# Performance work log

Measured on AMD Instinct MI355X. Metric: run time of the kernel, lower is better.

## Reference

```python
import jax, jax.numpy as jnp
import numpy as np

V, D, H, B, LK, LQ, PAD = 10000, 300, 512, 16, 64, 64, 0


def _lstm(x, Wih, Whh, b, h0, c0):
    # x: [B,T,D]; Wih: [4G,D]; Whh: [4G,G]; b: [4G] (b_ih+b_hh); torch gate order i,f,g,o
    xg = jnp.einsum('btd,gd->btg', x, Wih) + b
    def step(hc, xt):
        h, c = hc
        g = xt + h @ Whh.T
        i, f, gg, o = jnp.split(g, 4, axis=-1)
        c = jax.nn.sigmoid(f) * c + jax.nn.sigmoid(i) * jnp.tanh(gg)
        h = jax.nn.sigmoid(o) * jnp.tanh(c)
        return (h, c), h
    (hT, cT), hs = jax.lax.scan(step, (h0, c0), jnp.swapaxes(xg, 0, 1))
    return jnp.swapaxes(hs, 0, 1), hT, cT


def setup_inputs() -> dict:
    key = jax.random.key(0)
    ks = jax.random.split(key, 24)
    n = lambda k, s: (jax.random.normal(k, s, jnp.float32) * 0.05)
    return {
        'source': jax.random.randint(ks[0], (B, LK), 0, V),
        'prev_outputs': jax.random.randint(ks[1], (B, LQ), 0, V),
        'emb': n(ks[2], (V, D)),
        'enc_f_Wih': n(ks[3], (4 * H, D)), 'enc_f_Whh': n(ks[4], (4 * H, H)), 'enc_f_b': n(ks[5], (4 * H,)),
        'enc_b_Wih': n(ks[6], (4 * H, D)), 'enc_b_Whh': n(ks[7], (4 * H, H)), 'enc_b_b': n(ks[8], (4 * H,)),
        'dec_Wih': n(ks[9], (8 * H, D)), 'dec_Whh': n(ks[10], (8 * H, 2 * H)), 'dec_b': n(ks[11], (8 * H,)),
        'k_W': n(ks[12], (2 * H, 2 * H)), 'k_b': n(ks[13], (2 * H,)),
        'v_W': n(ks[14], (2 * H, 2 * H)), 'v_b': n(ks[15], (2 * H,)),
        'fc1_W': n(ks[16], (2 * H, 4 * H)), 'fc1_b': n(ks[17], (2 * H,)),
        'fc2_W': n(ks[18], (V, 2 * H)), 'fc2_b': n(ks[19], (V,)),
    }


def reference(source, prev_outputs, emb, enc_f_Wih, enc_f_Whh, enc_f_b,
              enc_b_Wih, enc_b_Whh, enc_b_b, dec_Wih, dec_Whh, dec_b,
              k_W, k_b, v_W, v_b, fc1_W, fc1_b, fc2_W, fc2_b):
    bsz = source.shape[0]
    xs = emb[source]  # [B,LK,300]
    z = jnp.zeros((bsz, H), xs.dtype)
    out_f, hf, cf = _lstm(xs, enc_f_Wih, enc_f_Whh, enc_f_b, z, z)
    out_b, hb, cb = _lstm(xs[:, ::-1], enc_b_Wih, enc_b_Whh, enc_b_b, z, z)
    enc_out = jnp.concatenate([out_f, out_b[:, ::-1]], axis=-1)  # [B,LK,1024]
    # self.change: interleave fwd/bwd channels -> [B,1024]
    h0 = jnp.stack([hf, hb], axis=-1).reshape(bsz, 2 * H)
    c0 = jnp.stack([cf, cb], axis=-1).reshape(bsz, 2 * H)
    Q, _, _ = _lstm(emb[prev_outputs], dec_Wih, dec_Whh, dec_b, h0, c0)  # [B,LQ,1024]
    K = enc_out @ k_W.T + k_b
    Vv = enc_out @ v_W.T + v_b
    M = jnp.einsum('bqc,bkc->bqk', Q, K)
    mask = (source == PAD)[:, None, :]
    M = jnp.where(mask, -jnp.inf, M)
    A = jax.nn.softmax(M, axis=2)
    ctx = jnp.einsum('bqk,bkc->bqc', A, Vv)  # == (A[...,None]*V[:,None]).sum(2)
    x = jnp.tanh(jnp.concatenate([ctx, Q], axis=-1) @ fc1_W.T + fc1_b)  # dropout=identity (eval)
    return x @ fc2_W.T + fc2_b
```

## Files before the change

kernel.cpp:

```cpp
#include <hip/hip_runtime.h>
#include <cmath>

#define BB   16
#define LKK  64
#define LQQ  64
#define DD   300
#define HH   512
#define H2   1024
#define G4   2048
#define G8   4096
#define VV   10000

__device__ __forceinline__ float sigmoidf_(float x) { return 1.f / (1.f + expf(-x)); }

typedef __attribute__((ext_vector_type(4))) float    f4_;
typedef __attribute__((ext_vector_type(4))) unsigned u4_;
typedef __attribute__((ext_vector_type(2))) unsigned u2_;

__device__ __forceinline__ void st_sc(float* p, float v) {
    __hip_atomic_store(p, v, __ATOMIC_RELAXED, __HIP_MEMORY_SCOPE_AGENT);
}

__device__ __forceinline__ f4_ ld4_sc(const float* p) {
    f4_ r;
    asm volatile("global_load_dwordx4 %0, %1, off sc0 sc1" : "=v"(r) : "v"(p));
    return r;
}
__device__ __forceinline__ u4_ ld4u_sc(const unsigned* p) {
    u4_ r;
    asm volatile("global_load_dwordx4 %0, %1, off sc0 sc1" : "=v"(r) : "v"(p));
    return r;
}
__device__ __forceinline__ u2_ ld2u_sc(const unsigned* p) {
    u2_ r;
    asm volatile("global_load_dwordx2 %0, %1, off sc0 sc1" : "=v"(r) : "v"(p));
    return r;
}
__device__ __forceinline__ void wait_vm0() {
    asm volatile("s_waitcnt vmcnt(0)" ::: "memory");
    __builtin_amdgcn_sched_barrier(0);
}
__device__ __forceinline__ void wait_vm1() {
    asm volatile("s_waitcnt vmcnt(1)" ::: "memory");
    __builtin_amdgcn_sched_barrier(0);
}

__device__ __forceinline__ void gbar256(unsigned* flags, int wg, unsigned target) {
    asm volatile("s_waitcnt vmcnt(0)" ::: "memory");
    if (threadIdx.x == 0)
        __hip_atomic_store(&flags[wg], target, __ATOMIC_RELAXED, __HIP_MEMORY_SCOPE_AGENT);
    if (threadIdx.x < 64) {
        const unsigned* p = flags + (threadIdx.x << 2);
        u4_ f0 = ld4u_sc(p);
        for (;;) {
            u4_ f1 = ld4u_sc(p);
            wait_vm1();
            unsigned m0 = f0[0] < f0[1] ? f0[0] : f0[1];
            unsigned m1 = f0[2] < f0[3] ? f0[2] : f0[3];
            if (__all((int)((m0 < m1 ? m0 : m1) >= target))) break;
            u4_ f2 = ld4u_sc(p);
            wait_vm1();
            m0 = f1[0] < f1[1] ? f1[0] : f1[1];
            m1 = f1[2] < f1[3] ? f1[2] : f1[3];
            if (__all((int)((m0 < m1 ? m0 : m1) >= target))) break;
            f0 = f2;
        }
        wait_vm0();
    }
    __syncthreads();
}

__device__ __forceinline__ void gbar128(unsigned* flags, int wg, unsigned target) {
    asm volatile("s_waitcnt vmcnt(0)" ::: "memory");
    if (threadIdx.x == 0)
        __hip_atomic_store(&flags[wg], target, __ATOMIC_RELAXED, __HIP_MEMORY_SCOPE_AGENT);
    if (threadIdx.x < 64) {
        const unsigned* p = flags + (threadIdx.x << 1);
        u2_ f0 = ld2u_sc(p);
        for (;;) {
            u2_ f1 = ld2u_sc(p);
            wait_vm1();
            unsigned mn = f0[0] < f0[1] ? f0[0] : f0[1];
            if (__all((int)(mn >= target))) break;
            u2_ f2 = ld2u_sc(p);
            wait_vm1();
            mn = f1[0] < f1[1] ? f1[0] : f1[1];
            if (__all((int)(mn >= target))) break;
            f0 = f2;
        }
        wait_vm0();
    }
    __syncthreads();
}

__global__ void rev_idx_kernel(const int* __restrict__ src, int* __restrict__ rev,
                               unsigned* __restrict__ bars) {
    int tid = blockIdx.x * blockDim.x + threadIdx.x;
    if (tid < 512) bars[tid] = 0u;
    if (tid < BB * LKK) {
        int b = tid / LKK, t = tid % LKK;
        rev[tid] = src[b * LKK + (LKK - 1 - t)];
    }
}

typedef __attribute__((ext_vector_type(8))) short bfrag8;
typedef __attribute__((ext_vector_type(4))) float facc4;

__device__ __forceinline__ unsigned short f2bf(float x) {
    unsigned u = __float_as_uint(x);
    unsigned r = (u + 0x7fffu + ((u >> 16) & 1u)) >> 16;
    return (unsigned short)r;
}

#define ASTR 40

__device__ __forceinline__ void gemm_core(
        short* __restrict__ Ah, short* __restrict__ Al,
        short* __restrict__ Bh, short* __restrict__ Bl,
        const float* __restrict__ A, const int* __restrict__ gidx, int lda,
        const float* __restrict__ Bw, int ldb,
        const float* __restrict__ bias,
        float* __restrict__ C, int ldc,
        int N, int K, int act, int m0, int n0) {
    int tid = threadIdx.x;
    int lane = tid & 63, w = tid >> 6;
    int wr = w >> 1, wc = w & 1;
    int fr = lane & 15, fg = lane >> 4;

    int sr = tid >> 1, sc = (tid & 1) << 4;
    long abase = gidx ? (long)gidx[m0 + sr] * lda : (long)(m0 + sr) * lda;
    int gn = n0 + sr;
    bool bval = gn < N;
    long bbase = (long)gn * ldb;

    facc4 acc[4][4] = {};

    for (int k0 = 0; k0 < K; k0 += 32) {
        {
            float v[16];
            if (k0 + sc + 16 <= K) {
                const float* ap = A + abase + k0 + sc;
                float4 t0 = *(const float4*)(ap + 0);
                float4 t1 = *(const float4*)(ap + 4);
                float4 t2 = *(const float4*)(ap + 8);
                float4 t3 = *(const float4*)(ap + 12);
                v[0]=t0.x; v[1]=t0.y; v[2]=t0.z;  v[3]=t0.w;
                v[4]=t1.x; v[5]=t1.y; v[6]=t1.z;  v[7]=t1.w;
                v[8]=t2.x; v[9]=t2.y; v[10]=t2.z; v[11]=t2.w;
                v[12]=t3.x; v[13]=t3.y; v[14]=t3.z; v[15]=t3.w;
            } else {
#pragma unroll
                for (int c = 0; c < 16; c++) {
                    int k = k0 + sc + c;
                    v[c] = (k < K) ? A[abase + k] : 0.f;
                }
            }
            bfrag8 h0, h1, l0, l1;
#pragma unroll
            for (int c = 0; c < 8; c++) {
                unsigned short hb = f2bf(v[c]);
                float hf = __uint_as_float(((unsigned)hb) << 16);
                h0[c] = (short)hb; l0[c] = (short)f2bf(v[c] - hf);
            }
#pragma unroll
            for (int c = 0; c < 8; c++) {
                unsigned short hb = f2bf(v[8 + c]);
                float hf = __uint_as_float(((unsigned)hb) << 16);
                h1[c] = (short)hb; l1[c] = (short)f2bf(v[8 + c] - hf);
            }
            *(bfrag8*)&Ah[sr * ASTR + sc]     = h0;
            *(bfrag8*)&Ah[sr * ASTR + sc + 8] = h1;
            *(bfrag8*)&Al[sr * ASTR + sc]     = l0;
            *(bfrag8*)&Al[sr * ASTR + sc + 8] = l1;
        }
        {
            float v[16];
            if (bval && (k0 + sc + 16 <= K)) {
                const float* bp = Bw + bbase + k0 + sc;
                float4 t0 = *(const float4*)(bp + 0);
                float4 t1 = *(const float4*)(bp + 4);
                float4 t2 = *(const float4*)(bp + 8);
                float4 t3 = *(const float4*)(bp + 12);
                v[0]=t0.x; v[1]=t0.y; v[2]=t0.z;  v[3]=t0.w;
                v[4]=t1.x; v[5]=t1.y; v[6]=t1.z;  v[7]=t1.w;
                v[8]=t2.x; v[9]=t2.y; v[10]=t2.z; v[11]=t2.w;
                v[12]=t3.x; v[13]=t3.y; v[14]=t3.z; v[15]=t3.w;
            } else {
#pragma unroll
                for (int c = 0; c < 16; c++) {
                    int k = k0 + sc + c;
                    v[c] = (bval && k < K) ? Bw[bbase + k] : 0.f;
                }
            }
            bfrag8 h0, h1, l0, l1;
#pragma unroll
            for (int c = 0; c < 8; c++) {
                unsigned short hb = f2bf(v[c]);
                float hf = __uint_as_float(((unsigned)hb) << 16);
                h0[c] = (short)hb; l0[c] = (short)f2bf(v[c] - hf);
            }
#pragma unroll
            for (int c = 0; c < 8; c++) {
                unsigned short hb = f2bf(v[8 + c]);
                float hf = __uint_as_float(((unsigned)hb) << 16);
                h1[c] = (short)hb; l1[c] = (short)f2bf(v[8 + c] - hf);
            }
            *(bfrag8*)&Bh[sr * ASTR + sc]     = h0;
            *(bfrag8*)&Bh[sr * ASTR + sc + 8] = h1;
            *(bfrag8*)&Bl[sr * ASTR + sc]     = l0;
            *(bfrag8*)&Bl[sr * ASTR + sc + 8] = l1;
        }
        __syncthreads();

        bfrag8 ah[4], al[4], bh[4], bl[4];
#pragma unroll
        for (int i = 0; i < 4; i++) {
            int ar = wr * 64 + i * 16 + fr;
            ah[i] = *(const bfrag8*)&Ah[ar * ASTR + fg * 8];
            al[i] = *(const bfrag8*)&Al[ar * ASTR + fg * 8];
            int br = wc * 64 + i * 16 + fr;
            bh[i] = *(const bfrag8*)&Bh[br * ASTR + fg * 8];
            bl[i] = *(const bfrag8*)&Bl[br * ASTR + fg * 8];
        }
#pragma unroll
        for (int i = 0; i < 4; i++)
#pragma unroll
            for (int j = 0; j < 4; j++) {
                acc[i][j] = __builtin_amdgcn_mfma_f32_16x16x32_bf16(ah[i], bh[j], acc[i][j], 0, 0, 0);
                acc[i][j] = __builtin_amdgcn_mfma_f32_16x16x32_bf16(ah[i], bl[j], acc[i][j], 0, 0, 0);
                acc[i][j] = __builtin_amdgcn_mfma_f32_16x16x32_bf16(al[i], bh[j], acc[i][j], 0, 0, 0);
            }
        __syncthreads();
    }

#pragma unroll
    for (int i = 0; i < 4; i++) {
        int row = m0 + wr * 64 + i * 16 + fg * 4;
#pragma unroll
        for (int j = 0; j < 4; j++) {
            int col = n0 + wc * 64 + j * 16 + fr;
            if (col < N) {
                float bz = bias[col];
#pragma unroll
                for (int q = 0; q < 4; q++) {
                    float vv = acc[i][j][q] + bz;
                    if (act == 1) vv = tanhf(vv);
                    C[(long)(row + q) * ldc + col] = vv;
                }
            }
        }
    }
}

__global__ __launch_bounds__(256)
void gemm_mfma128(const float* __restrict__ A, const int* __restrict__ gidx, int lda,
                  const float* __restrict__ Bw, int ldb,
                  const float* __restrict__ bias,
                  float* __restrict__ C, int ldc,
                  int N, int K, int act) {
    __shared__ __align__(16) short Ah[128 * ASTR];
    __shared__ __align__(16) short Al[128 * ASTR];
    __shared__ __align__(16) short Bh[128 * ASTR];
    __shared__ __align__(16) short Bl[128 * ASTR];
    gemm_core(Ah, Al, Bh, Bl, A, gidx, lda, Bw, ldb, bias, C, ldc, N, K, act,
              blockIdx.x * 128, blockIdx.y * 128);
}

__global__ __launch_bounds__(256)
void gemm_kv(const float* __restrict__ enc_out,
             const float* __restrict__ kW, const float* __restrict__ kb,
             const float* __restrict__ vW, const float* __restrict__ vb,
             float* __restrict__ Kbuf, float* __restrict__ Vbuf) {
    __shared__ __align__(16) short Ah[128 * ASTR];
    __shared__ __align__(16) short Al[128 * ASTR];
    __shared__ __align__(16) short Bh[128 * ASTR];
    __shared__ __align__(16) short Bl[128 * ASTR];
    int ny = blockIdx.y;
    if (ny < 8)
        gemm_core(Ah, Al, Bh, Bl, enc_out, nullptr, H2, kW, H2, kb, Kbuf, H2,
                  H2, H2, 0, blockIdx.x * 128, ny * 128);
    else
        gemm_core(Ah, Al, Bh, Bl, enc_out, nullptr, H2, vW, H2, vb, Vbuf, H2,
                  H2, H2, 0, blockIdx.x * 128, (ny - 8) * 128);
}

__global__ __launch_bounds__(256)
void gemm_xg(const float* __restrict__ emb,
             const int* __restrict__ src, const int* __restrict__ rev,
             const int* __restrict__ prev,
             const float* __restrict__ Wf, const float* __restrict__ bf,
             const float* __restrict__ Wb, const float* __restrict__ bb,
             const float* __restrict__ Wd, const float* __restrict__ bd,
             float* __restrict__ xf, float* __restrict__ xb,
             float* __restrict__ xd) {
    __shared__ __align__(16) short Ah[128 * ASTR];
    __shared__ __align__(16) short Al[128 * ASTR];
    __shared__ __align__(16) short Bh[128 * ASTR];
    __shared__ __align__(16) short Bl[128 * ASTR];
    int ny = blockIdx.y;
    if (ny < 16)
        gemm_core(Ah, Al, Bh, Bl, emb, src, DD, Wf, DD, bf, xf, G4,
                  G4, DD, 0, blockIdx.x * 128, ny * 128);
    else if (ny < 32)
        gemm_core(Ah, Al, Bh, Bl, emb, rev, DD, Wb, DD, bb, xb, G4,
                  G4, DD, 0, blockIdx.x * 128, (ny - 16) * 128);
    else
        gemm_core(Ah, Al, Bh, Bl, emb, prev, DD, Wd, DD, bd, xd, G8,
                  G8, DD, 0, blockIdx.x * 128, (ny - 32) * 128);
}

__global__ __launch_bounds__(256, 1)
void enc_recur(const float* __restrict__ xg_f, const float* __restrict__ xg_b,
               const float* __restrict__ Wf, const float* __restrict__ Wb,
               float* __restrict__ hglob, float* __restrict__ enc_out,
               float* __restrict__ encc, unsigned* __restrict__ flags) {
    __shared__ float hs[HH * 16];
    __shared__ float red[256 * 33];
    __shared__ float g256[256];
    __shared__ float hout[64];
    int wg  = blockIdx.x;
    int dir = wg >> 7;
    int j0  = (wg & 127) * 4;
    int tid = threadIdx.x;
    int ks   = tid & 31;
    int tile = tid >> 5;
    int bh   = tile >> 2;
    int gate = tile & 3;
    int sw   = (ks >> 2) & 3;
    const float* W  = dir ? Wb : Wf;
    const float* xg = dir ? xg_b : xg_f;
    unsigned* fl = flags + (dir << 7);
    int wgl = wg & 127;

    float wreg[4][16];
#pragma unroll
    for (int jn = 0; jn < 4; jn++) {
        const float* wrow = W + (long)(gate * HH + j0 + jn) * HH;
#pragma unroll
        for (int j = 0; j < 16; j++) wreg[jn][j] = wrow[ks + 32 * j];
    }

    int ub = tid & 15, ujj = tid >> 4;
    int xb = tid >> 4, xgate = (tid >> 2) & 3, xjn = tid & 3;
    float creg = 0.f;
    float4* hsv = (float4*)hs;

    for (int t = 0; t < LKK; t++) {
        float acc[8][4];
#pragma unroll
        for (int i = 0; i < 8; i++)
#pragma unroll
            for (int jn = 0; jn < 4; jn++) acc[i][jn] = 0.f;

        auto do_fma = [&](int jlo, int jhi) {
#pragma unroll
            for (int j = jlo; j < jhi; j++) {
                int k = ks + 32 * j;
                float4 h0 = hsv[k * 4 + ((bh * 2 + 0) ^ sw)];
                float4 h1 = hsv[k * 4 + ((bh * 2 + 1) ^ sw)];
#pragma unroll
                for (int jn = 0; jn < 4; jn++) {
                    float w = wreg[jn][j];
                    acc[0][jn] += h0.x * w; acc[1][jn] += h0.y * w;
                    acc[2][jn] += h0.z * w; acc[3][jn] += h0.w * w;
                    acc[4][jn] += h1.x * w; acc[5][jn] += h1.y * w;
                    acc[6][jn] += h1.z * w; acc[7][jn] += h1.w * w;
                }
            }
        };

        float xval = xg[(long)(xb * LKK + t) * G4 + xgate * HH + j0 + xjn];

        if (t == 0) {
            for (int i = tid; i < HH * 16; i += 256) hs[i] = 0.f;
            __syncthreads();
            do_fma(0, 16);
        } else {
            const float* hg = hglob + (long)((dir << 1) | (t & 1)) * (HH * 16);
            f4_ vv[8];
#pragma unroll
            for (int u = 0; u < 8; u++) vv[u] = ld4_sc(hg + tid * 4 + u * 1024);
            asm volatile("s_waitcnt vmcnt(4)" ::: "memory");
            __builtin_amdgcn_sched_barrier(0);
#pragma unroll
            for (int u = 0; u < 4; u++) {
                int e = tid * 4 + u * 1024;
                int jj = e >> 4, b0 = e & 15;
                *(f4_*)&hs[(jj << 4) + ((((b0 >> 2) ^ ((jj >> 2) & 3))) << 2)] = vv[u];
            }
            __syncthreads();
            do_fma(0, 8);
            wait_vm0();
#pragma unroll
            for (int u = 4; u < 8; u++) {
                int e = tid * 4 + u * 1024;
                int jj = e >> 4, b0 = e & 15;
                *(f4_*)&hs[(jj << 4) + ((((b0 >> 2) ^ ((jj >> 2) & 3))) << 2)] = vv[u];
            }
            __syncthreads();
            do_fma(8, 16);
        }

#pragma unroll
        for (int i = 0; i < 8; i++)
#pragma unroll
            for (int jn = 0; jn < 4; jn++)
                red[((bh * 8 + i) * 16 + gate * 4 + jn) * 33 + ks] = acc[i][jn];
        __syncthreads();
        {
            const float* row = red + tid * 33;
            float s0 = 0.f, s1 = 0.f, s2 = 0.f, s3 = 0.f;
#pragma unroll
            for (int u = 0; u < 8; u++) {
                s0 += row[u * 4 + 0]; s1 += row[u * 4 + 1];
                s2 += row[u * 4 + 2]; s3 += row[u * 4 + 3];
            }
            g256[tid] = ((s0 + s1) + (s2 + s3)) + xval;
        }
        __syncthreads();

        if (tid < 64) {
            int j = j0 + ujj;
            float gi = g256[ub * 16 + 0  + ujj];
            float gf = g256[ub * 16 + 4  + ujj];
            float gg = g256[ub * 16 + 8  + ujj];
            float go = g256[ub * 16 + 12 + ujj];
            float cv = sigmoidf_(gf) * creg + sigmoidf_(gi) * tanhf(gg);
            creg = cv;
            float hv = sigmoidf_(go) * tanhf(cv);
            st_sc(&hglob[(long)((dir << 1) | ((t + 1) & 1)) * (HH * 16) + j * 16 + ub], hv);
            hout[tid] = hv;
            if (t == LKK - 1) encc[(dir * BB + ub) * HH + j] = creg;
        }
        if (t < LKK - 1) gbar128(fl, wgl, (unsigned)(t + 1));
        else __syncthreads();
        if (tid >= 64 && tid < 128) {
            int lt = tid - 64;
            int j = j0 + (lt >> 4);
            int kpos = dir ? (LKK - 1 - t) : t;
            enc_out[(long)((lt & 15) * LKK + kpos) * H2 + dir * HH + j] = hout[lt];
        }
    }
}

__global__ __launch_bounds__(256, 1)
void dec_recur(const float* __restrict__ xg_d, const float* __restrict__ Wd,
               const float* __restrict__ enc_out, const float* __restrict__ encc,
               float* __restrict__ hglob, float* __restrict__ Qout,
               unsigned* __restrict__ flags) {
    __shared__ float hs[HH * 16];
    __shared__ float red[256 * 33];
    __shared__ float g256[256];
    __shared__ float hout[64];
    int wg  = blockIdx.x;
    int j0  = wg * 4;
    int tid = threadIdx.x;
    int ks   = tid & 31;
    int tile = tid >> 5;
    int bh   = tile >> 2;
    int gate = tile & 3;
    int sw   = (ks >> 2) & 3;

    float wreg[4][32];
#pragma unroll
    for (int jn = 0; jn < 4; jn++) {
        const float* wrow = Wd + (long)(gate * H2 + j0 + jn) * H2;
#pragma unroll
        for (int j = 0; j < 32; j++) wreg[jn][j] = wrow[ks + 32 * j];
    }

    int ub = tid & 15, ujj = tid >> 4;
    int xb = tid >> 4, xgate = (tid >> 2) & 3, xjn = tid & 3;
    float creg = 0.f;
    if (tid < 64) {
        int j = j0 + ujj;
        creg = ((j & 1) == 0) ? encc[ub * HH + (j >> 1)]
                              : encc[(BB + ub) * HH + (j >> 1)];
    }
    float4* hsv = (float4*)hs;

    for (int t = 0; t < LQQ; t++) {
        float xval = xg_d[(long)(xb * LQQ + t) * G8 + xgate * H2 + j0 + xjn];
        float acc[8][4];
#pragma unroll
        for (int i = 0; i < 8; i++)
#pragma unroll
            for (int jn = 0; jn < 4; jn++) acc[i][jn] = 0.f;

        auto do_fma = [&](int half) {
#pragma unroll
            for (int jj2 = 0; jj2 < 16; jj2++) {
                int j = half * 16 + jj2;
                int kl = ks + 32 * jj2;
                float4 h0 = hsv[kl * 4 + ((bh * 2 + 0) ^ sw)];
                float4 h1 = hsv[kl * 4 + ((bh * 2 + 1) ^ sw)];
#pragma unroll
                for (int jn = 0; jn < 4; jn++) {
                    float w = wreg[jn][j];
                    acc[0][jn] += h0.x * w; acc[1][jn] += h0.y * w;
                    acc[2][jn] += h0.z * w; acc[3][jn] += h0.w * w;
                    acc[4][jn] += h1.x * w; acc[5][jn] += h1.y * w;
                    acc[6][jn] += h1.z * w; acc[7][jn] += h1.w * w;
                }
            }
        };

        if (t == 0) {
            for (int half = 0; half < 2; half++) {
                for (int e = tid; e < HH * 16; e += 256) {
                    int kl = e >> 4, b = e & 15;
                    int k = half * HH + kl;
                    float hv = ((k & 1) == 0)
                        ? enc_out[(long)(b * LKK + (LKK - 1)) * H2 + (k >> 1)]
                        : enc_out[(long)(b * LKK) * H2 + HH + (k >> 1)];
                    hs[(kl << 4) + ((((b >> 2) ^ ((kl >> 2) & 3))) << 2) + (b & 3)] = hv;
                }
                __syncthreads();
                do_fma(half);
                __syncthreads();
            }
        } else {
            const float* hgA = hglob + (long)(t & 1) * (H2 * 16);
            f4_ vvA[8], vvB[8];
#pragma unroll
            for (int u = 0; u < 8; u++) vvA[u] = ld4_sc(hgA + tid * 4 + u * 1024);
#pragma unroll
            for (int u = 0; u < 8; u++) vvB[u] = ld4_sc(hgA + (HH * 16) + tid * 4 + u * 1024);
            asm volatile("s_waitcnt vmcnt(8)" ::: "memory");
            __builtin_amdgcn_sched_barrier(0);
#pragma unroll
            for (int u = 0; u < 8; u++) {
                int e = tid * 4 + u * 1024;
                int kl = e >> 4, b0 = e & 15;
                *(f4_*)&hs[(kl << 4) + ((((b0 >> 2) ^ ((kl >> 2) & 3))) << 2)] = vvA[u];
            }
            __syncthreads();
            do_fma(0);
            __syncthreads();
            wait_vm0();
#pragma unroll
            for (int u = 0; u < 8; u++) {
                int e = tid * 4 + u * 1024;
                int kl = e >> 4, b0 = e & 15;
                *(f4_*)&hs[(kl << 4) + ((((b0 >> 2) ^ ((kl >> 2) & 3))) << 2)] = vvB[u];
            }
            __syncthreads();
            do_fma(1);
        }

#pragma unroll
        for (int i = 0; i < 8; i++)
#pragma unroll
            for (int jn = 0; jn < 4; jn++)
                red[((bh * 8 + i) * 16 + gate * 4 + jn) * 33 + ks] = acc[i][jn];
        __syncthreads();
        {
            const float* row = red + tid * 33;
            float s0 = 0.f, s1 = 0.f, s2 = 0.f, s3 = 0.f;
#pragma unroll
            for (int u = 0; u < 8; u++) {
                s0 += row[u * 4 + 0]; s1 += row[u * 4 + 1];
                s2 += row[u * 4 + 2]; s3 += row[u * 4 + 3];
            }
            g256[tid] = ((s0 + s1) + (s2 + s3)) + xval;
        }
        __syncthreads();

        if (tid < 64) {
            int j = j0 + ujj;
            float gi = g256[ub * 16 + 0  + ujj];
            float gf = g256[ub * 16 + 4  + ujj];
            float gg = g256[ub * 16 + 8  + ujj];
            float go = g256[ub * 16 + 12 + ujj];
            float cv = sigmoidf_(gf) * creg + sigmoidf_(gi) * tanhf(gg);
            creg = cv;
            float hv = sigmoidf_(go) * tanhf(cv);
            st_sc(&hglob[(long)((t + 1) & 1) * (H2 * 16) + j * 16 + ub], hv);
            hout[tid] = hv;
        }
        if (t < LQQ - 1) gbar256(flags, wg, (unsigned)(t + 1));
        else __syncthreads();
        if (tid >= 64 && tid < 128) {
            int lt = tid - 64;
            int j = j0 + (lt >> 4);
            Qout[(long)((lt & 15) * LQQ + t) * H2 + j] = hout[lt];
        }
    }
}

__global__ __launch_bounds__(256)
void attention_kernel(const float* __restrict__ Qm, const float* __restrict__ Km,
                      const float* __restrict__ Vm, const int* __restrict__ source,
                      float* __restrict__ concatBuf) {
    int b = blockIdx.x >> 6;
    int q = blockIdx.x & 63;
    int tid = threadIdx.x;
    __shared__ float qrow[H2];
    __shared__ float part[LKK][4];
    __shared__ float aw[LKK];

    for (int i = tid; i < H2; i += 256) qrow[i] = Qm[(long)(b * LQQ + q) * H2 + i];
    __syncthreads();

    int k = tid >> 2, p = tid & 3;
    {
        const float* krow = Km + (long)(b * LKK + k) * H2 + p * 256;
        const float* qp = qrow + p * 256;
        float s = 0.f;
#pragma unroll 4
        for (int i = 0; i < 256; i++) s += qp[i] * krow[i];
        part[k][p] = s;
    }
    __syncthreads();
    if (tid < 64) {
        float sc = part[tid][0] + part[tid][1] + part[tid][2] + part[tid][3];
        bool masked = (source[b * LKK + tid] == 0);
        float m = masked ? -INFINITY : sc;
#pragma unroll
        for (int o = 32; o >= 1; o >>= 1) m = fmaxf(m, __shfl_xor(m, o, 64));
        float e = masked ? 0.f : expf(sc - m);
        float sum = e;
#pragma unroll
        for (int o = 32; o >= 1; o >>= 1) sum += __shfl_xor(sum, o, 64);
        aw[tid] = e / sum;
    }
    __syncthreads();

    for (int c = tid; c < H2; c += 256) {
        float acc = 0.f;
#pragma unroll 8
        for (int kk = 0; kk < LKK; kk++) acc += aw[kk] * Vm[(long)(b * LKK + kk) * H2 + c];
        long row = (long)(b * LQQ + q) * (2 * H2);
        concatBuf[row + c] = acc;
        concatBuf[row + H2 + c] = qrow[c];
    }
}

extern "C" void kernel_launch(void* const* d_in, const int* in_sizes, int n_in,
                              void* d_out, int out_size, void* d_ws, size_t ws_size,
                              hipStream_t stream) {
    const int*   src       = (const int*)  d_in[0];
    const int*   prev      = (const int*)  d_in[1];
    const float* emb       = (const float*)d_in[2];
    const float* enc_f_Wih = (const float*)d_in[3];
    const float* enc_f_Whh = (const float*)d_in[4];
    const float* enc_f_b   = (const float*)d_in[5];
    const float* enc_b_Wih = (const float*)d_in[6];
    const float* enc_b_Whh = (const float*)d_in[7];
    const float* enc_b_b   = (const float*)d_in[8];
    const float* dec_Wih   = (const float*)d_in[9];
    const float* dec_Whh   = (const float*)d_in[10];
    const float* dec_b     = (const float*)d_in[11];
    const float* k_W  = (const float*)d_in[12];
    const float* k_b  = (const float*)d_in[13];
    const float* v_W  = (const float*)d_in[14];
    const float* v_b  = (const float*)d_in[15];
    const float* fc1_W = (const float*)d_in[16];
    const float* fc1_b = (const float*)d_in[17];
    const float* fc2_W = (const float*)d_in[18];
    const float* fc2_b = (const float*)d_in[19];
    float* out = (float*)d_out;

    float* p = (float*)d_ws;
    float* xg_f    = p; p += (long)BB * LKK * G4;
    float* xg_b    = p; p += (long)BB * LKK * G4;
    float* xg_d    = p; p += (long)BB * LQQ * G8;
    float* enc_out = p; p += (long)BB * LKK * H2;
    float* encc    = p; p += 2L * BB * HH;
    float* hg_enc  = p; p += 2L * 2 * HH * 16;
    float* hg_dec  = p; p += 2L * H2 * 16;
    float* Qbuf    = p; p += (long)BB * LQQ * H2;
    float* Kbuf    = p; p += (long)BB * LKK * H2;
    float* Vbuf    = p; p += (long)BB * LKK * H2;
    float* concatB = p; p += (long)BB * LQQ * 2 * H2;
    float* fc1out  = p; p += (long)BB * LQQ * H2;
    int*   rev     = (int*)p; p += (BB * LKK);
    unsigned* bars = (unsigned*)p; p += 512;

    rev_idx_kernel<<<4, 256, 0, stream>>>(src, rev, bars);

    gemm_xg<<<dim3(8, 64), 256, 0, stream>>>(emb, src, rev, prev,
                                             enc_f_Wih, enc_f_b,
                                             enc_b_Wih, enc_b_b,
                                             dec_Wih, dec_b,
                                             xg_f, xg_b, xg_d);

    enc_recur<<<dim3(256), dim3(256), 0, stream>>>(xg_f, xg_b, enc_f_Whh, enc_b_Whh,
                                                   hg_enc, enc_out, encc, bars);

    gemm_kv<<<dim3(8, 16), 256, 0, stream>>>(enc_out, k_W, k_b, v_W, v_b, Kbuf, Vbuf);

    dec_recur<<<dim3(256), dim3(256), 0, stream>>>(xg_d, dec_Whh, enc_out, encc,
                                                   hg_dec, Qbuf, bars + 256);

    attention_kernel<<<BB * LQQ, 256, 0, stream>>>(Qbuf, Kbuf, Vbuf, src, concatB);

    gemm_mfma128<<<dim3(8, 8), 256, 0, stream>>>(concatB, nullptr, 2 * H2, fc1_W, 2 * H2,
                                                 fc1_b, fc1out, H2, H2, 2 * H2, 1);

    gemm_mfma128<<<dim3(8, (VV + 127) / 128), 256, 0, stream>>>(fc1out, nullptr, H2, fc2_W, H2,
                                                                fc2_b, out, VV, VV, H2, 0);
}
```

Measured before the change: 1.528 ms.

## Prefetch next GEMM K-tile into registers and add sleeping grid barrier

The split-bf16 MFMA GEMM core now loads the next 32-wide K slice of A and B into registers before converting and storing the current slice, so global load latency overlaps with LDS staging and MFMA work. The plain __syncthreads calls are replaced with an explicit lgkmcnt wait plus s_barrier. The decoder's 256-workgroup grid barrier drops its pipelined double-load polling loop in favour of a single load, a full wait and s_sleep between polls, which aims to cut memory traffic from spinning. The prefetch raises register pressure, and the sleep can add wake-up latency to each of the decoder's sequential barriers.

New measurement: 1.630 ms. +6.7%, slower.

```diff
diff --git a/kernel.cpp b/kernel.cpp
--- a/kernel.cpp
+++ b/kernel.cpp
@@ -45,27 +45,20 @@
     __builtin_amdgcn_sched_barrier(0);
 }
 
-__device__ __forceinline__ void gbar256(unsigned* flags, int wg, unsigned target) {
+__device__ __forceinline__ void gbar_slp(unsigned* flags, int wg, unsigned target) {
     asm volatile("s_waitcnt vmcnt(0)" ::: "memory");
     if (threadIdx.x == 0)
         __hip_atomic_store(&flags[wg], target, __ATOMIC_RELAXED, __HIP_MEMORY_SCOPE_AGENT);
     if (threadIdx.x < 64) {
-        const unsigned* p = flags + (threadIdx.x << 2);
-        u4_ f0 = ld4u_sc(p);
         for (;;) {
-            u4_ f1 = ld4u_sc(p);
-            wait_vm1();
-            unsigned m0 = f0[0] < f0[1] ? f0[0] : f0[1];
-            unsigned m1 = f0[2] < f0[3] ? f0[2] : f0[3];
-            if (__all((int)((m0 < m1 ? m0 : m1) >= target))) break;
-            u4_ f2 = ld4u_sc(p);
-            wait_vm1();
-            m0 = f1[0] < f1[1] ? f1[0] : f1[1];
-            m1 = f1[2] < f1[3] ? f1[2] : f1[3];
-            if (__all((int)((m0 < m1 ? m0 : m1) >= target))) break;
-            f0 = f2;
-        }
-        wait_vm0();
+            u4_ f = ld4u_sc(flags + (threadIdx.x << 2));
+            wait_vm0();
+            unsigned m0 = f[0] < f[1] ? f[0] : f[1];
+            unsigned m1 = f[2] < f[3] ? f[2] : f[3];
+            unsigned mn = m0 < m1 ? m0 : m1;
+            if (__all((int)(mn >= target))) break;
+            __builtin_amdgcn_s_sleep(1);
+        }
     }
     __syncthreads();
 }
@@ -111,6 +104,10 @@
     unsigned r = (u + 0x7fffu + ((u >> 16) & 1u)) >> 16;
     return (unsigned short)r;
 }
+__device__ __forceinline__ void lds_barrier() {
+    asm volatile("s_waitcnt lgkmcnt(0)" ::: "memory");
+    __builtin_amdgcn_s_barrier();
+}
 
 #define ASTR 40
 
@@ -135,38 +132,64 @@
 
     facc4 acc[4][4] = {};
 
+    auto loadt = [&](int k0v, float (&dva)[16], float (&dvb)[16]) {
+        if (k0v + sc + 16 <= K) {
+            const float* ap = A + abase + k0v + sc;
+            float4 t0 = *(const float4*)(ap + 0);
+            float4 t1 = *(const float4*)(ap + 4);
+            float4 t2 = *(const float4*)(ap + 8);
+            float4 t3 = *(const float4*)(ap + 12);
+            dva[0]=t0.x;  dva[1]=t0.y;  dva[2]=t0.z;  dva[3]=t0.w;
+            dva[4]=t1.x;  dva[5]=t1.y;  dva[6]=t1.z;  dva[7]=t1.w;
+            dva[8]=t2.x;  dva[9]=t2.y;  dva[10]=t2.z; dva[11]=t2.w;
+            dva[12]=t3.x; dva[13]=t3.y; dva[14]=t3.z; dva[15]=t3.w;
+        } else {
+#pragma unroll
+            for (int c = 0; c < 16; c++) {
+                int k = k0v + sc + c;
+                dva[c] = (k < K) ? A[abase + k] : 0.f;
+            }
+        }
+        if (bval && (k0v + sc + 16 <= K)) {
+            const float* bp = Bw + bbase + k0v + sc;
+            float4 t0 = *(const float4*)(bp + 0);
+            float4 t1 = *(const float4*)(bp + 4);
+            float4 t2 = *(const float4*)(bp + 8);
+            float4 t3 = *(const float4*)(bp + 12);
+            dvb[0]=t0.x;  dvb[1]=t0.y;  dvb[2]=t0.z;  dvb[3]=t0.w;
+            dvb[4]=t1.x;  dvb[5]=t1.y;  dvb[6]=t1.z;  dvb[7]=t1.w;
+            dvb[8]=t2.x;  dvb[9]=t2.y;  dvb[10]=t2.z; dvb[11]=t2.w;
+            dvb[12]=t3.x; dvb[13]=t3.y; dvb[14]=t3.z; dvb[15]=t3.w;
+        } else {
+#pragma unroll
+            for (int c = 0; c < 16; c++) {
+                int k = k0v + sc + c;
+                dvb[c] = (bval && k < K) ? Bw[bbase + k] : 0.f;
+            }
+        }
+    };
+
+    float va[16], vb[16];
+    loadt(0, va, vb);
+
     for (int k0 = 0; k0 < K; k0 += 32) {
+        float na[16], nb[16];
+        bool nxt = (k0 + 32) < K;
+        if (nxt) loadt(k0 + 32, na, nb);
+
         {
-            float v[16];
-            if (k0 + sc + 16 <= K) {
-                const float* ap = A + abase + k0 + sc;
-                float4 t0 = *(const float4*)(ap + 0);
-                float4 t1 = *(const float4*)(ap + 4);
-                float4 t2 = *(const float4*)(ap + 8);
-                float4 t3 = *(const float4*)(ap + 12);
-                v[0]=t0.x; v[1]=t0.y; v[2]=t0.z;  v[3]=t0.w;
-                v[4]=t1.x; v[5]=t1.y; v[6]=t1.z;  v[7]=t1.w;
-                v[8]=t2.x; v[9]=t2.y; v[10]=t2.z; v[11]=t2.w;
-                v[12]=t3.x; v[13]=t3.y; v[14]=t3.z; v[15]=t3.w;
-            } else {
-#pragma unroll
-                for (int c = 0; c < 16; c++) {
-                    int k = k0 + sc + c;
-                    v[c] = (k < K) ? A[abase + k] : 0.f;
-                }
-            }
             bfrag8 h0, h1, l0, l1;
 #pragma unroll
             for (int c = 0; c < 8; c++) {
-                unsigned short hb = f2bf(v[c]);
+                unsigned short hb = f2bf(va[c]);
                 float hf = __uint_as_float(((unsigned)hb) << 16);
-                h0[c] = (short)hb; l0[c] = (short)f2bf(v[c] - hf);
+                h0[c] = (short)hb; l0[c] = (short)f2bf(va[c] - hf);
             }
 #pragma unroll
             for (int c = 0; c < 8; c++) {
-                unsigned short hb = f2bf(v[8 + c]);
+                unsigned short hb = f2bf(va[8 + c]);
                 float hf = __uint_as_float(((unsigned)hb) << 16);
-                h1[c] = (short)hb; l1[c] = (short)f2bf(v[8 + c] - hf);
+                h1[c] = (short)hb; l1[c] = (short)f2bf(va[8 + c] - hf);
             }
             *(bfrag8*)&Ah[sr * ASTR + sc]     = h0;
             *(bfrag8*)&Ah[sr * ASTR + sc + 8] = h1;
@@ -174,43 +197,25 @@
             *(bfrag8*)&Al[sr * ASTR + sc + 8] = l1;
         }
         {
-            float v[16];
-            if (bval && (k0 + sc + 16 <= K)) {
-                const float* bp = Bw + bbase + k0 + sc;
-                float4 t0 = *(const float4*)(bp + 0);
-                float4 t1 = *(const float4*)(bp + 4);
-                float4 t2 = *(const float4*)(bp + 8);
-                float4 t3 = *(const float4*)(bp + 12);
-                v[0]=t0.x; v[1]=t0.y; v[2]=t0.z;  v[3]=t0.w;
-                v[4]=t1.x; v[5]=t1.y; v[6]=t1.z;  v[7]=t1.w;
-                v[8]=t2.x; v[9]=t2.y; v[10]=t2.z; v[11]=t2.w;
-                v[12]=t3.x; v[13]=t3.y; v[14]=t3.z; v[15]=t3.w;
-            } else {
-#pragma unroll
-                for (int c = 0; c < 16; c++) {
-                    int k = k0 + sc + c;
-                    v[c] = (bval && k < K) ? Bw[bbase + k] : 0.f;
-                }
-            }
             bfrag8 h0, h1, l0, l1;
 #pragma unroll
             for (int c = 0; c < 8; c++) {
-                unsigned short hb = f2bf(v[c]);
+                unsigned short hb = f2bf(vb[c]);
                 float hf = __uint_as_float(((unsigned)hb) << 16);
-                h0[c] = (short)hb; l0[c] = (short)f2bf(v[c] - hf);
+                h0[c] = (short)hb; l0[c] = (short)f2bf(vb[c] - hf);
             }
 #pragma unroll
             for (int c = 0; c < 8; c++) {
-                unsigned short hb = f2bf(v[8 + c]);
+                unsigned short hb = f2bf(vb[8 + c]);
                 float hf = __uint_as_float(((unsigned)hb) << 16);
-                h1[c] = (short)hb; l1[c] = (short)f2bf(v[8 + c] - hf);
+                h1[c] = (short)hb; l1[c] = (short)f2bf(vb[8 + c] - hf);
             }
             *(bfrag8*)&Bh[sr * ASTR + sc]     = h0;
             *(bfrag8*)&Bh[sr * ASTR + sc + 8] = h1;
             *(bfrag8*)&Bl[sr * ASTR + sc]     = l0;
             *(bfrag8*)&Bl[sr * ASTR + sc + 8] = l1;
         }
-        __syncthreads();
+        lds_barrier();
 
         bfrag8 ah[4], al[4], bh[4], bl[4];
 #pragma unroll
@@ -230,7 +235,12 @@
                 acc[i][j] = __builtin_amdgcn_mfma_f32_16x16x32_bf16(ah[i], bl[j], acc[i][j], 0, 0, 0);
                 acc[i][j] = __builtin_amdgcn_mfma_f32_16x16x32_bf16(al[i], bh[j], acc[i][j], 0, 0, 0);
             }
-        __syncthreads();
+        lds_barrier();
+
+        if (nxt) {
+#pragma unroll
+            for (int c = 0; c < 16; c++) { va[c] = na[c]; vb[c] = nb[c]; }
+        }
     }
 
 #pragma unroll
@@ -578,7 +588,7 @@
             st_sc(&hglob[(long)((t + 1) & 1) * (H2 * 16) + j * 16 + ub], hv);
             hout[tid] = hv;
         }
-        if (t < LQQ - 1) gbar256(flags, wg, (unsigned)(t + 1));
+        if (t < LQQ - 1) gbar_slp(flags, wg, (unsigned)(t + 1));
         else __syncthreads();
         if (tid >= 64 && tid < 128) {
             int lt = tid - 64;
```
